# Performance work log

Hardware: AMD Instinct MI355X
Metric: run time of the kernel (lower is better)

## Reference

```python
import jax, jax.numpy as jnp
import numpy as np

N_EMB = 512
DIM = 64
BETA = 0.25
EPS = 1e-10


def setup_inputs() -> dict:
    key = jax.random.key(0)
    k1, k2 = jax.random.split(key)
    z = jax.random.normal(k1, (32, 64, 64, 64), dtype=jnp.float32)  # (B, C=DIM, H, W)
    # embedding weight initialized uniform(-1/K, 1/K) as in the module
    weight = jax.random.uniform(k2, (N_EMB, DIM), dtype=jnp.float32,
                                minval=-1.0 / N_EMB, maxval=1.0 / N_EMB)
    return {"z": z, "weight": weight}


def reference(z, weight):
    # (B,C,H,W) -> (B,H,W,C)
    zp = jnp.transpose(z, (0, 2, 3, 1))
    zf = zp.reshape(-1, DIM)  # (N, D)
    # pairwise squared distances ||z||^2 + ||e||^2 - 2 z.e  -> (N, K)
    d = (jnp.sum(zf * zf, axis=1, keepdims=True)
         + jnp.sum(weight * weight, axis=1)
         - 2.0 * zf @ weight.T)
    codebook = jnp.argmin(d, axis=1)  # (N,)
    encodings = jax.nn.one_hot(codebook, N_EMB, dtype=zf.dtype)  # (N, K)
    # direct gather == one_hot @ weight (same math, efficient form)
    z_q = weight[codebook].reshape(zp.shape)
    sg = jax.lax.stop_gradient
    loss = jnp.mean((sg(z_q) - zp) ** 2) + BETA * jnp.mean((z_q - sg(zp)) ** 2)
    # straight-through estimator
    z_q = zp + sg(z_q - zp)
    e_mean = jnp.mean(encodings, axis=0)
    perplexity = jnp.exp(-jnp.sum(e_mean * jnp.log(e_mean + EPS)))
    z_q = jnp.transpose(z_q, (0, 3, 1, 2))  # back to (B,C,H,W)
    return (loss, z_q, perplexity, encodings, codebook)
```

## Files before the change

kernel.cpp:

```cpp
#include <hip/hip_runtime.h>
#include <math.h>

#define NK 512
#define NPTS (32*64*64)
#define NELEM (32*64*64*64)

#define OFF_LOSS 0
#define OFF_ZQ   1
#define OFF_PERP (1 + NELEM)
#define OFF_ENC  (2 + NELEM)
#define OFF_CB   (2 + NELEM + (size_t)NPTS * NK)

typedef float v2f __attribute__((ext_vector_type(2)));


__global__ __launch_bounds__(256) void vq_prep(const float* __restrict__ wg,
                                               float* __restrict__ wT,
                                               float* __restrict__ bnd) {
    __shared__ float tl[64 * 65];
    const int t = threadIdx.x;
    const int kbase = blockIdx.x * 64;
    #pragma unroll
    for (int it = 0; it < 16; ++it) {
        int i = it * 256 + t;
        int k = i >> 6, d = i & 63;
        tl[k * 65 + d] = wg[(size_t)(kbase + k) * 64 + d];
    }
    __syncthreads();
    #pragma unroll
    for (int it = 0; it < 16; ++it) {
        int j = it * 256 + t;
        int d = j >> 6, kk = j & 63;
        wT[(size_t)d * 512 + kbase + kk] = tl[kk * 65 + d];
    }
    if (t < 64) {
        float s = 0.f;
        #pragma unroll 4
        for (int d = 0; d < 64; ++d) {
            float v = tl[t * 65 + d];
            s = __fadd_rn(s, __fmul_rn(v, v));
        }
        bnd[kbase + t] = s;
    }
}

__global__ __launch_bounds__(256, 2) void vq_main(const float* __restrict__ zg,
                                                  const float* __restrict__ wg,
                                                  const float* __restrict__ wT,
                                                  const float* __restrict__ bndg,
                                                  float* __restrict__ out,
                                                  int* __restrict__ hist,
                                                  double* __restrict__ lossAcc) {
    const int t = threadIdx.x;
    const int blk = blockIdx.x;
    const int b = blk >> 6;
    const int h = blk & 63;

    __shared__ __align__(16) float zt[64 * 64];
    __shared__ __align__(16) float buf[4096];
    __shared__ __align__(16) float r2v[256];
    __shared__ int   r2i[256];
    __shared__ float aRow[64];
    __shared__ int   idxs[64];
    __shared__ float wsum[4];

    float* redv = buf;
    int*   redi = (int*)(buf + 2048);
    float* zqt  = buf;

    {
        const size_t base = (size_t)b * 262144 + (size_t)h * 64;
        const int w2 = (t & 31) * 2;
        const int c0 = t >> 5;
        #pragma unroll
        for (int c = c0; c < 64; c += 8) {
            float2 v = *(const float2*)(zg + base + (size_t)c * 4096 + w2);
            *(float2*)(zt + c * 64 + w2) = v;
        }
    }
    __syncthreads();

    if (t < 64) {
        float s = 0.f;
        for (int d = 0; d < 64; ++d) {
            float v = zt[d * 64 + t];
            s = __fadd_rn(s, __fmul_rn(v, v));
        }
        aRow[t] = s;
    }

    {
        float4* enc = (float4*)(out + OFF_ENC + (size_t)blk * 64 * NK);
        const float4 zv4 = make_float4(0.f, 0.f, 0.f, 0.f);
        #pragma unroll
        for (int it = 0; it < 32; ++it)
            enc[(size_t)it * 256 + t] = zv4;
    }
    __syncthreads();

    const int tx = t & 7;
    const int ty = t >> 3;
    const int p0 = tx * 8;
    const int k0 = ty * 8;

    float best[8];
    int bidx[8];
    #pragma unroll
    for (int i = 0; i < 8; ++i) { best[i] = INFINITY; bidx[i] = 0; }

    const float* ztp = zt + p0;

    #pragma unroll
    for (int c = 0; c < 2; ++c) {
        v2f acc[8][4];
        #pragma unroll
        for (int i = 0; i < 8; ++i)
            #pragma unroll
            for (int jj = 0; jj < 4; ++jj) acc[i][jj] = (v2f){0.f, 0.f};

        const float* wrow = wT + c * 256 + k0;

        #pragma unroll 4
        for (int d = 0; d < 64; ++d) {
            float4 z0 = *(const float4*)(ztp + d * 64);
            float4 z1 = *(const float4*)(ztp + d * 64 + 4);
            float4 w0 = *(const float4*)(wrow + d * 512);
            float4 w1 = *(const float4*)(wrow + d * 512 + 4);
            const float zr[8] = {z0.x, z0.y, z0.z, z0.w, z1.x, z1.y, z1.z, z1.w};
            v2f wv[4];
            wv[0] = (v2f){w0.x, w0.y}; wv[1] = (v2f){w0.z, w0.w};
            wv[2] = (v2f){w1.x, w1.y}; wv[3] = (v2f){w1.z, w1.w};
            #pragma unroll
            for (int i = 0; i < 8; ++i) {
                v2f zz = (v2f){zr[i], zr[i]};
                #pragma unroll
                for (int jj = 0; jj < 4; ++jj)
                    acc[i][jj] = __builtin_elementwise_fma(zz, wv[jj], acc[i][jj]);
            }
        }

        float bn[8];
        {
            const float4* bp = (const float4*)(bndg + c * 256 + k0);
            float4 b0 = bp[0], b1 = bp[1];
            bn[0] = b0.x; bn[1] = b0.y; bn[2] = b0.z; bn[3] = b0.w;
            bn[4] = b1.x; bn[5] = b1.y; bn[6] = b1.z; bn[7] = b1.w;
        }
        float av[8];
        {
            float4 a0 = *(const float4*)(aRow + p0);
            float4 a1 = *(const float4*)(aRow + p0 + 4);
            av[0] = a0.x; av[1] = a0.y; av[2] = a0.z; av[3] = a0.w;
            av[4] = a1.x; av[5] = a1.y; av[6] = a1.z; av[7] = a1.w;
        }

        #pragma unroll
        for (int i = 0; i < 8; ++i) {
            #pragma unroll
            for (int j = 0; j < 8; ++j) {
                float dotv = acc[i][j >> 1][j & 1];
                float dist = __fsub_rn(__fadd_rn(av[i], bn[j]), 2.0f * dotv);
                int k = c * 256 + k0 + j;
                if (dist < best[i]) { best[i] = dist; bidx[i] = k; }
            }
        }
    }
    __syncthreads();

    #pragma unroll
    for (int i = 0; i < 8; ++i) {
        redv[ty * 64 + p0 + i] = best[i];
        redi[ty * 64 + p0 + i] = bidx[i];
    }
    __syncthreads();

    {
        const int p = t & 63, g = t >> 6;
        float bv = INFINITY; int bi = 0;
        #pragma unroll
        for (int x = g * 8; x < g * 8 + 8; ++x) {
            float v = redv[x * 64 + p];
            int ii = redi[x * 64 + p];
            if (v < bv || (v == bv && ii < bi)) { bv = v; bi = ii; }
        }
        r2v[g * 64 + p] = bv;
        r2i[g * 64 + p] = bi;
    }
    __syncthreads();

    if (t < 64) {
        float bv = r2v[t];
        int bi = r2i[t];
        #pragma unroll
        for (int g = 1; g < 4; ++g) {
            float v = r2v[g * 64 + t];
            int ii = r2i[g * 64 + t];
            if (v < bv || (v == bv && ii < bi)) { bv = v; bi = ii; }
        }
        idxs[t] = bi;
        atomicAdd(&hist[bi], 1);
        out[OFF_CB + (size_t)blk * 64 + t] = (float)bi;
        out[OFF_ENC + (size_t)blk * 64 * NK + (size_t)t * NK + bi] = 1.0f;
    }
    __syncthreads();

    if (t < 128) {
        const int p = t >> 1, half = t & 1;
        const int bi = idxs[p];
        const float4* wr4 = (const float4*)(wg + (size_t)bi * 64) + half * 8;
        #pragma unroll
        for (int q = 0; q < 8; ++q) {
            float4 v = wr4[q];
            int d = half * 32 + q * 4;
            zqt[(d + 0) * 64 + p] = v.x;
            zqt[(d + 1) * 64 + p] = v.y;
            zqt[(d + 2) * 64 + p] = v.z;
            zqt[(d + 3) * 64 + p] = v.w;
        }
    }
    __syncthreads();

    float lsum = 0.f;
    {
        float* zq = out + OFF_ZQ + (size_t)b * 262144 + (size_t)h * 64;
        #pragma unroll
        for (int it = 0; it < 4; ++it) {
            int f = it * 256 + t;
            int d = f >> 4, pp = (f & 15) * 4;
            float4 zv = *(const float4*)(zt + d * 64 + pp);
            float4 qv = *(const float4*)(zqt + d * 64 + pp);
            float4 o;
            float dx = __fsub_rn(qv.x, zv.x); lsum = __fadd_rn(lsum, __fmul_rn(dx, dx)); o.x = __fadd_rn(zv.x, dx);
            float dy = __fsub_rn(qv.y, zv.y); lsum = __fadd_rn(lsum, __fmul_rn(dy, dy)); o.y = __fadd_rn(zv.y, dy);
            float dz = __fsub_rn(qv.z, zv.z); lsum = __fadd_rn(lsum, __fmul_rn(dz, dz)); o.z = __fadd_rn(zv.z, dz);
            float dw = __fsub_rn(qv.w, zv.w); lsum = __fadd_rn(lsum, __fmul_rn(dw, dw)); o.w = __fadd_rn(zv.w, dw);
            *(float4*)(zq + (size_t)d * 4096 + pp) = o;
        }
    }
    #pragma unroll
    for (int off = 32; off > 0; off >>= 1)
        lsum += __shfl_down(lsum, off);
    if ((t & 63) == 0) wsum[t >> 6] = lsum;
    __syncthreads();
    if (t == 0) {
        float tot = (wsum[0] + wsum[1]) + (wsum[2] + wsum[3]);
        atomicAdd(lossAcc, (double)tot);
    }
}

__global__ __launch_bounds__(512) void vq_finalize(const int* __restrict__ hist,
                                                   const double* __restrict__ lossAcc,
                                                   float* __restrict__ out) {
    __shared__ float sh[512];
    const int t = threadIdx.x;
    float p = (float)hist[t] / (float)NPTS;
    sh[t] = __fmul_rn(p, logf(__fadd_rn(p, 1e-10f)));
    __syncthreads();
    for (int s = 256; s > 0; s >>= 1) {
        if (t < s) sh[t] += sh[t + s];
        __syncthreads();
    }
    if (t == 0) {
        float m = (float)(*lossAcc / (double)NELEM);
        out[OFF_LOSS] = __fadd_rn(m, __fmul_rn(0.25f, m));
        out[OFF_PERP] = expf(-sh[0]);
    }
}

extern "C" void kernel_launch(void* const* d_in, const int* in_sizes, int n_in,
                              void* d_out, int out_size, void* d_ws, size_t ws_size,
                              hipStream_t stream) {
    const float* z = (const float*)d_in[0];
    const float* w = (const float*)d_in[1];
    float* out = (float*)d_out;
    int* hist = (int*)d_ws;
    double* lossAcc = (double*)((char*)d_ws + 2048);
    float* wT = (float*)((char*)d_ws + 4096);
    float* bnd = wT + 64 * 512;

    (void)hipMemsetAsync(d_ws, 0, 4096, stream);
    vq_prep<<<8, 256, 0, stream>>>(w, wT, bnd);
    vq_main<<<2048, 256, 0, stream>>>(z, w, wT, bnd, out, hist, lossAcc);
    vq_finalize<<<1, 512, 0, stream>>>(hist, lossAcc, out);
}
```

Before: 439.5 us.

## Shrink per-thread tile and LDS footprint to raise vq_main occupancy

```diff
diff --git a/kernel.cpp b/kernel.cpp
--- a/kernel.cpp
+++ b/kernel.cpp
@@ -44,7 +44,7 @@
     }
 }
 
-__global__ __launch_bounds__(256, 2) void vq_main(const float* __restrict__ zg,
+__global__ __launch_bounds__(256, 6) void vq_main(const float* __restrict__ zg,
                                                   const float* __restrict__ wg,
                                                   const float* __restrict__ wT,
                                                   const float* __restrict__ bndg,
@@ -57,16 +57,15 @@
     const int h = blk & 63;
 
     __shared__ __align__(16) float zt[64 * 64];
-    __shared__ __align__(16) float buf[4096];
     __shared__ __align__(16) float r2v[256];
     __shared__ int   r2i[256];
     __shared__ float aRow[64];
     __shared__ int   idxs[64];
     __shared__ float wsum[4];
 
-    float* redv = buf;
-    int*   redi = (int*)(buf + 2048);
-    float* zqt  = buf;
+    float* redv = zt;
+    int*   redi = (int*)(zt + 1024);
+    float* zqt  = zt;
 
     {
         const size_t base = (size_t)b * 262144 + (size_t)h * 64;
@@ -98,40 +97,45 @@
     }
     __syncthreads();
 
-    const int tx = t & 7;
-    const int ty = t >> 3;
-    const int p0 = tx * 8;
-    const int k0 = ty * 8;
-
-    float best[8];
-    int bidx[8];
-    #pragma unroll
-    for (int i = 0; i < 8; ++i) { best[i] = INFINITY; bidx[i] = 0; }
+    const int pg = t & 15;
+    const int cg = t >> 4;
+    const int p0 = pg * 4;
+    const int k0 = cg * 8;
+
+    float best[4];
+    int bidx[4];
+    #pragma unroll
+    for (int i = 0; i < 4; ++i) { best[i] = INFINITY; bidx[i] = 0; }
+
+    float av[4];
+    {
+        float4 a0 = *(const float4*)(aRow + p0);
+        av[0] = a0.x; av[1] = a0.y; av[2] = a0.z; av[3] = a0.w;
+    }
 
     const float* ztp = zt + p0;
 
     #pragma unroll
-    for (int c = 0; c < 2; ++c) {
-        v2f acc[8][4];
-        #pragma unroll
-        for (int i = 0; i < 8; ++i)
+    for (int c = 0; c < 4; ++c) {
+        v2f acc[4][4];
+        #pragma unroll
+        for (int i = 0; i < 4; ++i)
             #pragma unroll
             for (int jj = 0; jj < 4; ++jj) acc[i][jj] = (v2f){0.f, 0.f};
 
-        const float* wrow = wT + c * 256 + k0;
+        const float* wbase = wT + c * 128 + k0;
 
         #pragma unroll 4
         for (int d = 0; d < 64; ++d) {
-            float4 z0 = *(const float4*)(ztp + d * 64);
-            float4 z1 = *(const float4*)(ztp + d * 64 + 4);
-            float4 w0 = *(const float4*)(wrow + d * 512);
-            float4 w1 = *(const float4*)(wrow + d * 512 + 4);
-            const float zr[8] = {z0.x, z0.y, z0.z, z0.w, z1.x, z1.y, z1.z, z1.w};
+            float4 z4 = *(const float4*)(ztp + d * 64);
+            float4 w0 = *(const float4*)(wbase + d * 512);
+            float4 w1 = *(const float4*)(wbase + d * 512 + 4);
             v2f wv[4];
             wv[0] = (v2f){w0.x, w0.y}; wv[1] = (v2f){w0.z, w0.w};
             wv[2] = (v2f){w1.x, w1.y}; wv[3] = (v2f){w1.z, w1.w};
+            const float zr[4] = {z4.x, z4.y, z4.z, z4.w};
             #pragma unroll
-            for (int i = 0; i < 8; ++i) {
+            for (int i = 0; i < 4; ++i) {
                 v2f zz = (v2f){zr[i], zr[i]};
                 #pragma unroll
                 for (int jj = 0; jj < 4; ++jj)
@@ -141,26 +145,19 @@
 
         float bn[8];
         {
-            const float4* bp = (const float4*)(bndg + c * 256 + k0);
+            const float4* bp = (const float4*)(bndg + c * 128 + k0);
             float4 b0 = bp[0], b1 = bp[1];
             bn[0] = b0.x; bn[1] = b0.y; bn[2] = b0.z; bn[3] = b0.w;
             bn[4] = b1.x; bn[5] = b1.y; bn[6] = b1.z; bn[7] = b1.w;
         }
-        float av[8];
-        {
-            float4 a0 = *(const float4*)(aRow + p0);
-            float4 a1 = *(const float4*)(aRow + p0 + 4);
-            av[0] = a0.x; av[1] = a0.y; av[2] = a0.z; av[3] = a0.w;
-            av[4] = a1.x; av[5] = a1.y; av[6] = a1.z; av[7] = a1.w;
-        }
-
-        #pragma unroll
-        for (int i = 0; i < 8; ++i) {
+
+        #pragma unroll
+        for (int i = 0; i < 4; ++i) {
             #pragma unroll
             for (int j = 0; j < 8; ++j) {
                 float dotv = acc[i][j >> 1][j & 1];
                 float dist = __fsub_rn(__fadd_rn(av[i], bn[j]), 2.0f * dotv);
-                int k = c * 256 + k0 + j;
+                int k = c * 128 + k0 + j;
                 if (dist < best[i]) { best[i] = dist; bidx[i] = k; }
             }
         }
@@ -168,9 +165,9 @@
     __syncthreads();
 
     #pragma unroll
-    for (int i = 0; i < 8; ++i) {
-        redv[ty * 64 + p0 + i] = best[i];
-        redi[ty * 64 + p0 + i] = bidx[i];
+    for (int i = 0; i < 4; ++i) {
+        redv[cg * 64 + p0 + i] = best[i];
+        redi[cg * 64 + p0 + i] = bidx[i];
     }
     __syncthreads();
 
@@ -178,7 +175,7 @@
         const int p = t & 63, g = t >> 6;
         float bv = INFINITY; int bi = 0;
         #pragma unroll
-        for (int x = g * 8; x < g * 8 + 8; ++x) {
+        for (int x = g * 4; x < g * 4 + 4; ++x) {
             float v = redv[x * 64 + p];
             int ii = redi[x * 64 + p];
             if (v < bv || (v == bv && ii < bi)) { bv = v; bi = ii; }
@@ -222,12 +219,14 @@
 
     float lsum = 0.f;
     {
-        float* zq = out + OFF_ZQ + (size_t)b * 262144 + (size_t)h * 64;
+        const size_t base = (size_t)b * 262144 + (size_t)h * 64;
+        const float* zrow = zg + base;
+        float* zq = out + OFF_ZQ + base;
         #pragma unroll
         for (int it = 0; it < 4; ++it) {
             int f = it * 256 + t;
             int d = f >> 4, pp = (f & 15) * 4;
-            float4 zv = *(const float4*)(zt + d * 64 + pp);
+            float4 zv = *(const float4*)(zrow + (size_t)d * 4096 + pp);
             float4 qv = *(const float4*)(zqt + d * 64 + pp);
             float4 o;
             float dx = __fsub_rn(qv.x, zv.x); lsum = __fadd_rn(lsum, __fmul_rn(dx, dx)); o.x = __fadd_rn(zv.x, dx);
```

Result: slower. 610.0 us (+38.8%).
